# Optimization experiments

Hardware: AMD Instinct MI355X
Metric: run time of the kernel (lower is better)

Reference implementation:

```python
import jax, jax.numpy as jnp
import numpy as np
import math

B, SES, SEQ, H, K = 16, 16, 64, 512, 32
L = SES * SEQ


def setup_inputs() -> dict:
    key = jax.random.key(0)
    ks = jax.random.split(key, 16)
    s = 1.0 / math.sqrt(H)
    return {
        "user_emb": jax.random.normal(ks[0], (B, H), jnp.float32),
        "item_emb": jax.random.normal(ks[1], (B, SES, SEQ, H), jnp.float32),
        "mask": jnp.zeros((B, L, K), jnp.float32),
        "index": jax.random.randint(ks[2], (L, K), 0, L, jnp.int64),
        "Wq": jax.random.normal(ks[3], (H, H), jnp.float32) * s,
        "bq": jnp.zeros((H,), jnp.float32),
        "Wk": jax.random.normal(ks[4], (H, H), jnp.float32) * s,
        "bk": jnp.zeros((H,), jnp.float32),
        "Wv": jax.random.normal(ks[5], (H, H), jnp.float32) * s,
        "bv": jnp.zeros((H,), jnp.float32),
        "Wd": jax.random.normal(ks[6], (H, H), jnp.float32) * s,
        "bd": jnp.zeros((H,), jnp.float32),
        "ln_g": jnp.ones((H,), jnp.float32),
        "ln_b": jnp.zeros((H,), jnp.float32),
    }


def reference(user_emb, item_emb, mask, index, Wq, bq, Wk, bk, Wv, bv, Wd, bd, ln_g, ln_b):
    b, ses, seq, h = item_emb.shape
    l = ses * seq
    item_flat = item_emb.reshape(b, l, h)
    q = user_emb @ Wq.T + bq                       # [B, H]
    k = item_flat @ Wk.T + bk                      # [B, L, H]
    v = item_flat @ Wv.T + bv                      # [B, L, H]
    # scalar query against all L keys, scaled by sqrt(hidden_size)
    scores = jnp.einsum("bh,blh->bl", q, k) / math.sqrt(h)
    scores = scores[:, index] + mask               # gather -> [B, L, K]
    w = jax.nn.softmax(scores, axis=-1)            # [B, L, K]
    vg = v[:, index, :]                            # gather -> [B, L, K, H]
    attn_out = jnp.einsum("blk,blkh->blh", w, vg)  # [B, L, H]
    dense = attn_out @ Wd.T + bd
    x = dense + item_flat                          # residual (dropout = identity, eval)
    mu = jnp.mean(x, axis=-1, keepdims=True)
    var = jnp.var(x, axis=-1, keepdims=True)
    y = (x - mu) / jnp.sqrt(var + 1e-12) * ln_g + ln_b
    return y.reshape(b, ses, seq, h)
```

## Files before the change

kernel.cpp:

```cpp
#include <hip/hip_runtime.h>
#include <math.h>

constexpr int HD   = 512;
constexpr int LL   = 1024;
constexpr int MT   = 16384;
constexpr int KNBR = 32;
constexpr float SCL = 0.04419417382415922f;

typedef __attribute__((ext_vector_type(8))) short  bf16x8;
typedef __attribute__((ext_vector_type(4))) float  f32x4;

__device__ inline float b2f(unsigned short u) {
    union { unsigned int i; float f; } v; v.i = (unsigned int)u << 16; return v.f;
}
__device__ inline float b2f_lo(unsigned int u) {
    union { unsigned int i; float f; } v; v.i = u << 16; return v.f;
}
__device__ inline float b2f_hi(unsigned int u) {
    union { unsigned int i; float f; } v; v.i = u & 0xffff0000u; return v.f;
}
__device__ inline unsigned short f2b(float x) {
    union { float f; unsigned int u; } v; v.f = x;
    unsigned int r = v.u + 0x7fff + ((v.u >> 16) & 1);
    return (unsigned short)(r >> 16);
}

constexpr int PB_CONV_I = 8192;
constexpr int PB_CONV_W = 512;
constexpr int PB_Q      = 2048;

__global__ __launch_bounds__(256) void prep(
    const float* __restrict__ item, const float* __restrict__ Wv,
    const float* __restrict__ Wd, const float* __restrict__ u,
    const float* __restrict__ Wq, const float* __restrict__ bq,
    unsigned short* __restrict__ item_bf, unsigned short* __restrict__ Wv_bf,
    unsigned short* __restrict__ Wd_bf, float* __restrict__ q)
{
    const int blk = blockIdx.x, tid = threadIdx.x;

    if (blk < PB_CONV_I) {
        const int i = blk * 1024 + tid * 4;
        float4 v = *(const float4*)&item[i];
        ushort4 o;
        o.x = f2b(v.x); o.y = f2b(v.y); o.z = f2b(v.z); o.w = f2b(v.w);
        *(ushort4*)&item_bf[i] = o;
        return;
    }
    if (blk < PB_CONV_I + PB_CONV_W) {
        const int n = HD*HD;
        const int i = (blk - PB_CONV_I) * 1024 + tid * 4;
        const float* s; unsigned short* d; int off;
        if (i < n) { s = Wv; d = Wv_bf; off = i; }
        else       { s = Wd; d = Wd_bf; off = i - n; }
        float4 v = *(const float4*)&s[off];
        ushort4 o;
        o.x = f2b(v.x); o.y = f2b(v.y); o.z = f2b(v.z); o.w = f2b(v.w);
        *(ushort4*)&d[off] = o;
        return;
    }
    {
        const int wid  = (blk - PB_CONV_I - PB_CONV_W) * 4 + (tid >> 6);
        const int lane = tid & 63;
        const int b = wid >> 9, h = wid & 511;
        const float* ur = &u[b*HD + lane*8];
        const float* wr = &Wq[(size_t)h*HD + lane*8];
        const float4 u0 = *(const float4*)ur, u1 = *(const float4*)(ur+4);
        const float4 w0 = *(const float4*)wr, w1 = *(const float4*)(wr+4);
        float acc = u0.x*w0.x + u0.y*w0.y + u0.z*w0.z + u0.w*w0.w
                  + u1.x*w1.x + u1.y*w1.y + u1.z*w1.z + u1.w*w1.w;
        #pragma unroll
        for (int off = 32; off; off >>= 1) acc += __shfl_down(acc, off);
        if (lane == 0) q[b*HD + h] = acc + bq[h];
    }
}

__global__ __launch_bounds__(256) void gemm_v_r(
    const unsigned short* __restrict__ A, const unsigned short* __restrict__ W,
    const float* __restrict__ bv, const float* __restrict__ Wk,
    const float* __restrict__ bk, const float* __restrict__ q,
    unsigned short* __restrict__ v_bf, float* __restrict__ rbuf,
    float* __restrict__ s0buf)
{
    __shared__ unsigned short As[128 * 32];
    __shared__ unsigned short Bs[128 * 32];

    const int blk = blockIdx.x;
    const int tid = threadIdx.x;

    if (blk >= 512) {
        if (blk < 640) {
            __shared__ float red[4][64];
            const int rblk = blk - 512;
            const int b = rblk >> 3, c0 = (rblk & 7) * 64;
            const int cl = tid & 63, hg = tid >> 6;
            const float* qb = &q[b*HD];
            const float* wb = &Wk[(size_t)hg*128*HD + c0 + cl];
            float acc = 0.f;
            #pragma unroll 8
            for (int h = 0; h < 128; h++)
                acc += qb[hg*128 + h] * wb[(size_t)h*HD];
            red[hg][cl] = acc;
            __syncthreads();
            if (tid < 64)
                rbuf[b*HD + c0 + tid] = SCL *
                    (red[0][tid] + red[1][tid] + red[2][tid] + red[3][tid]);
        } else {
            __shared__ float sp[4];
            const int b = blk - 640;
            float p = q[b*HD + tid]*bk[tid] + q[b*HD + tid + 256]*bk[tid + 256];
            #pragma unroll
            for (int off = 32; off; off >>= 1) p += __shfl_down(p, off);
            if ((tid & 63) == 0) sp[tid >> 6] = p;
            __syncthreads();
            if (tid == 0) s0buf[b] = (sp[0] + sp[1] + sp[2] + sp[3]) * SCL;
        }
        return;
    }

    const int wave = tid >> 6, lane = tid & 63;
    const int wm = (wave >> 1) * 64;
    const int wn = (wave & 1)  * 64;
    const int row0 = (blk >> 2) * 128;
    const int col0 = (blk & 3)  * 128;

    const int lrr = lane >> 2;
    const int cc  = lane & 3;
    int st_row[2], st_gchunk[2];
    #pragma unroll
    for (int t = 0; t < 2; t++) {
        const int m = wave*32 + t*16 + lrr;
        st_row[t]    = m;
        st_gchunk[t] = cc ^ ((m >> 1) & 3);
    }

    const int fr   = lane & 15;
    const int quad = lane >> 4;

    f32x4 acc[4][4];
    #pragma unroll
    for (int i = 0; i < 4; i++)
        #pragma unroll
        for (int j = 0; j < 4; j++)
            acc[i][j] = (f32x4){0.f, 0.f, 0.f, 0.f};

    int a_off[4], b_off[4];
    #pragma unroll
    for (int i = 0; i < 4; i++) {
        const int m = wm + i*16 + fr;
        a_off[i] = m*32 + ((quad ^ ((m >> 1) & 3)) << 3);
        const int n = wn + i*16 + fr;
        b_off[i] = n*32 + ((quad ^ ((n >> 1) & 3)) << 3);
    }

    for (int k0 = 0; k0 < HD; k0 += 32) {
        #pragma unroll
        for (int t = 0; t < 2; t++) {
            const int m = st_row[t];
            const unsigned short* ga = &A[(size_t)(row0 + m)*HD + k0 + st_gchunk[t]*8];
            __builtin_amdgcn_global_load_lds(
                (const __attribute__((address_space(1))) void*)ga,
                (__attribute__((address_space(3))) void*)&As[(wave*32 + t*16)*32],
                16, 0, 0);
            const unsigned short* gw = &W[(size_t)(col0 + m)*HD + k0 + st_gchunk[t]*8];
            __builtin_amdgcn_global_load_lds(
                (const __attribute__((address_space(1))) void*)gw,
                (__attribute__((address_space(3))) void*)&Bs[(wave*32 + t*16)*32],
                16, 0, 0);
        }
        __syncthreads();

        bf16x8 af[4], bfr[4];
        #pragma unroll
        for (int i = 0; i < 4; i++) {
            af[i]  = *(const bf16x8*)&As[a_off[i]];
            bfr[i] = *(const bf16x8*)&Bs[b_off[i]];
        }
        #pragma unroll
        for (int i = 0; i < 4; i++)
            #pragma unroll
            for (int j = 0; j < 4; j++)
                acc[i][j] = __builtin_amdgcn_mfma_f32_16x16x32_bf16(
                    af[i], bfr[j], acc[i][j], 0, 0, 0);
        __syncthreads();
    }

    #pragma unroll
    for (int j = 0; j < 4; j++) {
        const int col = col0 + wn + j*16 + fr;
        const float bb = bv[col];
        #pragma unroll
        for (int i = 0; i < 4; i++) {
            #pragma unroll
            for (int r = 0; r < 4; r++) {
                const int row = row0 + wm + i*16 + quad*4 + r;
                v_bf[(size_t)row*HD + col] = f2b(acc[i][j][r] + bb);
            }
        }
    }
}

__global__ __launch_bounds__(256) void gp_scores(
    const float* __restrict__ rbuf, const float* __restrict__ s0buf,
    const unsigned short* __restrict__ item_bf, float* __restrict__ scores)
{
    const int m = blockIdx.x * 4 + (threadIdx.x >> 6);
    const int lane = threadIdx.x & 63;
    const int b = m >> 10;
    const unsigned short* ir = &item_bf[(size_t)m*HD + lane*8];
    const uint4 iv = *(const uint4*)ir;
    const float* rr = &rbuf[b*HD + lane*8];
    const float4 r0 = *(const float4*)rr;
    const float4 r1 = *(const float4*)(rr + 4);
    float acc = r0.x*b2f_lo(iv.x) + r0.y*b2f_hi(iv.x)
              + r0.z*b2f_lo(iv.y) + r0.w*b2f_hi(iv.y)
              + r1.x*b2f_lo(iv.z) + r1.y*b2f_hi(iv.z)
              + r1.z*b2f_lo(iv.w) + r1.w*b2f_hi(iv.w);
    #pragma unroll
    for (int off = 32; off; off >>= 1) acc += __shfl_down(acc, off);
    if (lane == 0) scores[m] = acc + s0buf[b];
}

__global__ __launch_bounds__(256) void gp_attn(
    const float* __restrict__ scores, const int* __restrict__ index,
    const float* __restrict__ mask, const unsigned short* __restrict__ v,
    unsigned short* __restrict__ attn)
{
    const int m = blockIdx.x * 4 + (threadIdx.x >> 6);
    const int lane = threadIdx.x & 63;
    const int b = m >> 10, l = m & 1023;

    const int t = lane & 31;
    const int idx = index[l*KNBR + t];
    const float s = scores[b*LL + idx] + mask[(size_t)m*KNBR + t];

    float mx = s;
    #pragma unroll
    for (int off = 16; off; off >>= 1) mx = fmaxf(mx, __shfl_xor(mx, off));
    const float e = __expf(s - mx);
    float sum = e;
    #pragma unroll
    for (int off = 16; off; off >>= 1) sum += __shfl_xor(sum, off);
    const float w = e / sum;

    const unsigned short* vbase = v + (size_t)(b << 10) * HD + lane*8;
    float a[8] = {};
    #pragma unroll 8
    for (int t2 = 0; t2 < KNBR; t2++) {
        const int   it = __shfl(idx, t2);
        const float wt = __shfl(w,   t2);
        const uint4 pv = *(const uint4*)(vbase + (size_t)it*HD);
        a[0] += wt * b2f_lo(pv.x); a[1] += wt * b2f_hi(pv.x);
        a[2] += wt * b2f_lo(pv.y); a[3] += wt * b2f_hi(pv.y);
        a[4] += wt * b2f_lo(pv.z); a[5] += wt * b2f_hi(pv.z);
        a[6] += wt * b2f_lo(pv.w); a[7] += wt * b2f_hi(pv.w);
    }
    uint4 o;
    o.x = (unsigned int)f2b(a[0]) | ((unsigned int)f2b(a[1]) << 16);
    o.y = (unsigned int)f2b(a[2]) | ((unsigned int)f2b(a[3]) << 16);
    o.z = (unsigned int)f2b(a[4]) | ((unsigned int)f2b(a[5]) << 16);
    o.w = (unsigned int)f2b(a[6]) | ((unsigned int)f2b(a[7]) << 16);
    *(uint4*)&attn[(size_t)m*HD + lane*8] = o;
}

__global__ __launch_bounds__(256) void dense_ln(
    const unsigned short* __restrict__ A,
    const unsigned short* __restrict__ W,
    const float* __restrict__ bd, const unsigned short* __restrict__ res,
    const float* __restrict__ ln_g, const float* __restrict__ ln_b,
    float* __restrict__ out)
{
    __shared__ unsigned short As[32 * 32];
    __shared__ unsigned short Bs[512 * 32];
    __shared__ float g_s[HD], lb_s[HD];
    __shared__ float rsum[4][32], rsq[4][32];

    const int tid  = threadIdx.x;
    const int wave = tid >> 6, lane = tid & 63;
    const int row0 = blockIdx.x * 32;

    {
        const int i = tid * 2;
        *(float2*)&g_s[i]  = *(const float2*)&ln_g[i];
        *(float2*)&lb_s[i] = *(const float2*)&ln_b[i];
    }

    const int lrr = lane >> 2;
    const int cc  = lane & 3;
    const int fr   = lane & 15;
    const int quad = lane >> 4;

    f32x4 acc[2][8];
    #pragma unroll
    for (int i = 0; i < 2; i++)
        #pragma unroll
        for (int j = 0; j < 8; j++)
            acc[i][j] = (f32x4){0.f, 0.f, 0.f, 0.f};

    int a_off[2], b_off[8];
    #pragma unroll
    for (int i = 0; i < 2; i++) {
        const int m = i*16 + fr;
        a_off[i] = m*32 + ((quad ^ ((m >> 1) & 3)) << 3);
    }
    #pragma unroll
    for (int j = 0; j < 8; j++) {
        const int n = wave*128 + j*16 + fr;
        b_off[j] = n*32 + ((quad ^ ((n >> 1) & 3)) << 3);
    }

    for (int k0 = 0; k0 < HD; k0 += 32) {
        #pragma unroll
        for (int t = 0; t < 8; t++) {
            const int n = wave*128 + t*16 + lrr;
            const int gch = cc ^ ((n >> 1) & 3);
            const unsigned short* gw = &W[(size_t)n*HD + k0 + gch*8];
            __builtin_amdgcn_global_load_lds(
                (const __attribute__((address_space(1))) void*)gw,
                (__attribute__((address_space(3))) void*)&Bs[(wave*128 + t*16)*32],
                16, 0, 0);
        }
        if (wave < 2) {
            const int m = wave*16 + lrr;
            const int gch = cc ^ ((m >> 1) & 3);
            const unsigned short* ga = &A[(size_t)(row0 + m)*HD + k0 + gch*8];
            __builtin_amdgcn_global_load_lds(
                (const __attribute__((address_space(1))) void*)ga,
                (__attribute__((address_space(3))) void*)&As[(wave*16)*32],
                16, 0, 0);
        }
        __syncthreads();

        bf16x8 af[2], bfr[8];
        #pragma unroll
        for (int i = 0; i < 2; i++) af[i] = *(const bf16x8*)&As[a_off[i]];
        #pragma unroll
        for (int j = 0; j < 8; j++) bfr[j] = *(const bf16x8*)&Bs[b_off[j]];
        #pragma unroll
        for (int i = 0; i < 2; i++)
            #pragma unroll
            for (int j = 0; j < 8; j++)
                acc[i][j] = __builtin_amdgcn_mfma_f32_16x16x32_bf16(
                    af[i], bfr[j], acc[i][j], 0, 0, 0);
        __syncthreads();
    }

    float bdv[8];
    #pragma unroll
    for (int j = 0; j < 8; j++) bdv[j] = bd[wave*128 + j*16 + fr];

    #pragma unroll
    for (int i = 0; i < 2; i++) {
        #pragma unroll
        for (int r = 0; r < 4; r++) {
            const int lrow = i*16 + quad*4 + r;
            const size_t gr = (size_t)(row0 + lrow) * HD;
            float a1 = 0.f, a2 = 0.f;
            #pragma unroll
            for (int j = 0; j < 8; j++) {
                const int col = wave*128 + j*16 + fr;
                float val = acc[i][j][r] + bdv[j] + b2f(res[gr + col]);
                acc[i][j][r] = val;
                a1 += val; a2 += val*val;
            }
            #pragma unroll
            for (int off = 1; off < 16; off <<= 1) {
                a1 += __shfl_xor(a1, off);
                a2 += __shfl_xor(a2, off);
            }
            if (fr == 0) { rsum[wave][lrow] = a1; rsq[wave][lrow] = a2; }
        }
    }
    __syncthreads();

    #pragma unroll
    for (int i = 0; i < 2; i++) {
        #pragma unroll
        for (int r = 0; r < 4; r++) {
            const int lrow = i*16 + quad*4 + r;
            const float tot  = rsum[0][lrow] + rsum[1][lrow] + rsum[2][lrow] + rsum[3][lrow];
            const float tot2 = rsq[0][lrow]  + rsq[1][lrow]  + rsq[2][lrow]  + rsq[3][lrow];
            const float mu  = tot * (1.f/HD);
            const float var = tot2 * (1.f/HD) - mu*mu;
            const float inv = rsqrtf(var + 1e-12f);
            const size_t gr = (size_t)(row0 + lrow) * HD;
            #pragma unroll
            for (int j = 0; j < 8; j++) {
                const int col = wave*128 + j*16 + fr;
                out[gr + col] = (acc[i][j][r] - mu)*inv*g_s[col] + lb_s[col];
            }
        }
    }
}

extern "C" void kernel_launch(void* const* d_in, const int* in_sizes, int n_in,
                              void* d_out, int out_size, void* d_ws, size_t ws_size,
                              hipStream_t stream) {
    const float* user_emb = (const float*)d_in[0];
    const float* item_emb = (const float*)d_in[1];
    const float* mask     = (const float*)d_in[2];
    const int*   index    = (const int*)  d_in[3];
    const float* Wq = (const float*)d_in[4];  const float* bq = (const float*)d_in[5];
    const float* Wk = (const float*)d_in[6];  const float* bk = (const float*)d_in[7];
    const float* Wv = (const float*)d_in[8];  const float* bv = (const float*)d_in[9];
    const float* Wd = (const float*)d_in[10]; const float* bd = (const float*)d_in[11];
    const float* ln_g = (const float*)d_in[12];
    const float* ln_b = (const float*)d_in[13];

    float* out = (float*)d_out;

    char* p = (char*)d_ws;
    unsigned short* item_bf = (unsigned short*)p; p += (size_t)MT*HD*2;
    unsigned short* v_bf    = (unsigned short*)p; p += (size_t)MT*HD*2;
    unsigned short* attn_bf = (unsigned short*)p; p += (size_t)MT*HD*2;
    unsigned short* Wv_bf   = (unsigned short*)p; p += (size_t)HD*HD*2;
    unsigned short* Wd_bf   = (unsigned short*)p; p += (size_t)HD*HD*2;
    float* q      = (float*)p; p += 16*HD*4;
    float* rbuf   = (float*)p; p += 16*HD*4;
    float* s0buf  = (float*)p; p += 16*4;
    float* scores = (float*)p; p += MT*4;

    prep<<<PB_CONV_I + PB_CONV_W + PB_Q, 256, 0, stream>>>(
        item_emb, Wv, Wd, user_emb, Wq, bq,
        item_bf, Wv_bf, Wd_bf, q);

    gemm_v_r<<<656, 256, 0, stream>>>(item_bf, Wv_bf, bv, Wk, bk, q,
                                      v_bf, rbuf, s0buf);

    gp_scores<<<MT/4, 256, 0, stream>>>(rbuf, s0buf, item_bf, scores);

    gp_attn<<<MT/4, 256, 0, stream>>>(scores, index, mask, v_bf, attn_bf);

    dense_ln<<<MT/32, 256, 0, stream>>>(attn_bf, Wd_bf, bd, item_bf,
                                        ln_g, ln_b, out);
}
```

Baseline: 192.4 us.

## Double-buffer GEMM LDS tiles, remap block order, widen dense_ln tile

Both bf16 GEMMs (V projection and dense+LayerNorm) now double-buffer their LDS tiles, so the next k-slice is loaded while MFMAs run on the current one, with one barrier per iteration. Block indices in gemm_v_r and gp_attn are permuted so that concurrently scheduled blocks spread across batches and row groups, which changes cache and channel locality. dense_ln now uses 512 threads on 64-row tiles, halving how often the full Wd panel is restaged per output row, and reads LN gamma/beta straight into registers. The cost is more LDS per block (about 72KB in dense_ln), which can limit occupancy.

```diff
diff --git a/kernel.cpp b/kernel.cpp
--- a/kernel.cpp
+++ b/kernel.cpp
@@ -81,8 +81,8 @@
     unsigned short* __restrict__ v_bf, float* __restrict__ rbuf,
     float* __restrict__ s0buf)
 {
-    __shared__ unsigned short As[128 * 32];
-    __shared__ unsigned short Bs[128 * 32];
+    __shared__ unsigned short As[2][128 * 32];
+    __shared__ unsigned short Bs[2][128 * 32];
 
     const int blk = blockIdx.x;
     const int tid = threadIdx.x;
@@ -117,11 +117,14 @@
         return;
     }
 
+    const int rowb = (blk & 7) | ((blk >> 5) << 3);
+    const int colb = (blk >> 3) & 3;
+    const int row0 = rowb * 128;
+    const int col0 = colb * 128;
+
     const int wave = tid >> 6, lane = tid & 63;
     const int wm = (wave >> 1) * 64;
     const int wn = (wave & 1)  * 64;
-    const int row0 = (blk >> 2) * 128;
-    const int col0 = (blk & 3)  * 128;
 
     const int lrr = lane >> 2;
     const int cc  = lane & 3;
@@ -152,28 +155,34 @@
         b_off[i] = n*32 + ((quad ^ ((n >> 1) & 3)) << 3);
     }
 
-    for (int k0 = 0; k0 < HD; k0 += 32) {
+    auto stage = [&](int bf, int k0) {
         #pragma unroll
         for (int t = 0; t < 2; t++) {
             const int m = st_row[t];
             const unsigned short* ga = &A[(size_t)(row0 + m)*HD + k0 + st_gchunk[t]*8];
             __builtin_amdgcn_global_load_lds(
                 (const __attribute__((address_space(1))) void*)ga,
-                (__attribute__((address_space(3))) void*)&As[(wave*32 + t*16)*32],
+                (__attribute__((address_space(3))) void*)&As[bf][(wave*32 + t*16)*32],
                 16, 0, 0);
             const unsigned short* gw = &W[(size_t)(col0 + m)*HD + k0 + st_gchunk[t]*8];
             __builtin_amdgcn_global_load_lds(
                 (const __attribute__((address_space(1))) void*)gw,
-                (__attribute__((address_space(3))) void*)&Bs[(wave*32 + t*16)*32],
+                (__attribute__((address_space(3))) void*)&Bs[bf][(wave*32 + t*16)*32],
                 16, 0, 0);
         }
-        __syncthreads();
+    };
+
+    stage(0, 0);
+    __syncthreads();
+    int cur = 0;
+    for (int k0 = 0; k0 < HD; k0 += 32) {
+        if (k0 + 32 < HD) stage(cur ^ 1, k0 + 32);
 
         bf16x8 af[4], bfr[4];
         #pragma unroll
         for (int i = 0; i < 4; i++) {
-            af[i]  = *(const bf16x8*)&As[a_off[i]];
-            bfr[i] = *(const bf16x8*)&Bs[b_off[i]];
+            af[i]  = *(const bf16x8*)&As[cur][a_off[i]];
+            bfr[i] = *(const bf16x8*)&Bs[cur][b_off[i]];
         }
         #pragma unroll
         for (int i = 0; i < 4; i++)
@@ -182,6 +191,7 @@
                 acc[i][j] = __builtin_amdgcn_mfma_f32_16x16x32_bf16(
                     af[i], bfr[j], acc[i][j], 0, 0, 0);
         __syncthreads();
+        cur ^= 1;
     }
 
     #pragma unroll
@@ -225,7 +235,8 @@
     const float* __restrict__ mask, const unsigned short* __restrict__ v,
     unsigned short* __restrict__ attn)
 {
-    const int m = blockIdx.x * 4 + (threadIdx.x >> 6);
+    const int bid = blockIdx.x;
+    const int m = ((bid & 7) << 11) | ((bid >> 3) << 2) | (int)(threadIdx.x >> 6);
     const int lane = threadIdx.x & 63;
     const int b = m >> 10, l = m & 1023;
 
@@ -262,102 +273,103 @@
     *(uint4*)&attn[(size_t)m*HD + lane*8] = o;
 }
 
-__global__ __launch_bounds__(256) void dense_ln(
+__global__ __launch_bounds__(512) void dense_ln(
     const unsigned short* __restrict__ A,
     const unsigned short* __restrict__ W,
     const float* __restrict__ bd, const unsigned short* __restrict__ res,
     const float* __restrict__ ln_g, const float* __restrict__ ln_b,
     float* __restrict__ out)
 {
-    __shared__ unsigned short As[32 * 32];
-    __shared__ unsigned short Bs[512 * 32];
-    __shared__ float g_s[HD], lb_s[HD];
-    __shared__ float rsum[4][32], rsq[4][32];
+    __shared__ unsigned short As[2][64 * 32];
+    __shared__ unsigned short Bs[2][512 * 32];
+    __shared__ float rsum[8][64], rsq[8][64];
 
     const int tid  = threadIdx.x;
     const int wave = tid >> 6, lane = tid & 63;
-    const int row0 = blockIdx.x * 32;
-
-    {
-        const int i = tid * 2;
-        *(float2*)&g_s[i]  = *(const float2*)&ln_g[i];
-        *(float2*)&lb_s[i] = *(const float2*)&ln_b[i];
-    }
+    const int row0 = blockIdx.x * 64;
 
     const int lrr = lane >> 2;
     const int cc  = lane & 3;
     const int fr   = lane & 15;
     const int quad = lane >> 4;
 
-    f32x4 acc[2][8];
-    #pragma unroll
-    for (int i = 0; i < 2; i++)
-        #pragma unroll
-        for (int j = 0; j < 8; j++)
+    f32x4 acc[4][4];
+    #pragma unroll
+    for (int i = 0; i < 4; i++)
+        #pragma unroll
+        for (int j = 0; j < 4; j++)
             acc[i][j] = (f32x4){0.f, 0.f, 0.f, 0.f};
 
-    int a_off[2], b_off[8];
-    #pragma unroll
-    for (int i = 0; i < 2; i++) {
+    int a_off[4], b_off[4];
+    #pragma unroll
+    for (int i = 0; i < 4; i++) {
         const int m = i*16 + fr;
         a_off[i] = m*32 + ((quad ^ ((m >> 1) & 3)) << 3);
-    }
-    #pragma unroll
-    for (int j = 0; j < 8; j++) {
-        const int n = wave*128 + j*16 + fr;
-        b_off[j] = n*32 + ((quad ^ ((n >> 1) & 3)) << 3);
-    }
-
-    for (int k0 = 0; k0 < HD; k0 += 32) {
-        #pragma unroll
-        for (int t = 0; t < 8; t++) {
-            const int n = wave*128 + t*16 + lrr;
+        const int n = wave*64 + i*16 + fr;
+        b_off[i] = n*32 + ((quad ^ ((n >> 1) & 3)) << 3);
+    }
+
+    auto stage = [&](int bf, int k0) {
+        #pragma unroll
+        for (int t = 0; t < 4; t++) {
+            const int n   = t*128 + wave*16 + lrr;
             const int gch = cc ^ ((n >> 1) & 3);
             const unsigned short* gw = &W[(size_t)n*HD + k0 + gch*8];
             __builtin_amdgcn_global_load_lds(
                 (const __attribute__((address_space(1))) void*)gw,
-                (__attribute__((address_space(3))) void*)&Bs[(wave*128 + t*16)*32],
+                (__attribute__((address_space(3))) void*)&Bs[bf][(t*128 + wave*16)*32],
                 16, 0, 0);
         }
-        if (wave < 2) {
-            const int m = wave*16 + lrr;
-            const int gch = cc ^ ((m >> 1) & 3);
-            const unsigned short* ga = &A[(size_t)(row0 + m)*HD + k0 + gch*8];
+        if (wave < 4) {
+            const int mm  = wave*16 + lrr;
+            const int gch = cc ^ ((mm >> 1) & 3);
+            const unsigned short* ga = &A[(size_t)(row0 + mm)*HD + k0 + gch*8];
             __builtin_amdgcn_global_load_lds(
                 (const __attribute__((address_space(1))) void*)ga,
-                (__attribute__((address_space(3))) void*)&As[(wave*16)*32],
+                (__attribute__((address_space(3))) void*)&As[bf][(wave*16)*32],
                 16, 0, 0);
         }
-        __syncthreads();
-
-        bf16x8 af[2], bfr[8];
-        #pragma unroll
-        for (int i = 0; i < 2; i++) af[i] = *(const bf16x8*)&As[a_off[i]];
-        #pragma unroll
-        for (int j = 0; j < 8; j++) bfr[j] = *(const bf16x8*)&Bs[b_off[j]];
-        #pragma unroll
-        for (int i = 0; i < 2; i++)
-            #pragma unroll
-            for (int j = 0; j < 8; j++)
+    };
+
+    stage(0, 0);
+    __syncthreads();
+    int cur = 0;
+    for (int k0 = 0; k0 < HD; k0 += 32) {
+        if (k0 + 32 < HD) stage(cur ^ 1, k0 + 32);
+
+        bf16x8 af[4], bfr[4];
+        #pragma unroll
+        for (int i = 0; i < 4; i++) {
+            af[i]  = *(const bf16x8*)&As[cur][a_off[i]];
+            bfr[i] = *(const bf16x8*)&Bs[cur][b_off[i]];
+        }
+        #pragma unroll
+        for (int i = 0; i < 4; i++)
+            #pragma unroll
+            for (int j = 0; j < 4; j++)
                 acc[i][j] = __builtin_amdgcn_mfma_f32_16x16x32_bf16(
                     af[i], bfr[j], acc[i][j], 0, 0, 0);
         __syncthreads();
-    }
-
-    float bdv[8];
-    #pragma unroll
-    for (int j = 0; j < 8; j++) bdv[j] = bd[wave*128 + j*16 + fr];
-
-    #pragma unroll
-    for (int i = 0; i < 2; i++) {
+        cur ^= 1;
+    }
+
+    float bdv[4], gv[4], lbv[4];
+    #pragma unroll
+    for (int j = 0; j < 4; j++) {
+        const int col = wave*64 + j*16 + fr;
+        bdv[j] = bd[col]; gv[j] = ln_g[col]; lbv[j] = ln_b[col];
+    }
+
+    #pragma unroll
+    for (int i = 0; i < 4; i++) {
         #pragma unroll
         for (int r = 0; r < 4; r++) {
             const int lrow = i*16 + quad*4 + r;
             const size_t gr = (size_t)(row0 + lrow) * HD;
             float a1 = 0.f, a2 = 0.f;
             #pragma unroll
-            for (int j = 0; j < 8; j++) {
-                const int col = wave*128 + j*16 + fr;
+            for (int j = 0; j < 4; j++) {
+                const int col = wave*64 + j*16 + fr;
                 float val = acc[i][j][r] + bdv[j] + b2f(res[gr + col]);
                 acc[i][j][r] = val;
                 a1 += val; a2 += val*val;
@@ -373,20 +385,24 @@
     __syncthreads();
 
     #pragma unroll
-    for (int i = 0; i < 2; i++) {
+    for (int i = 0; i < 4; i++) {
         #pragma unroll
         for (int r = 0; r < 4; r++) {
             const int lrow = i*16 + quad*4 + r;
-            const float tot  = rsum[0][lrow] + rsum[1][lrow] + rsum[2][lrow] + rsum[3][lrow];
-            const float tot2 = rsq[0][lrow]  + rsq[1][lrow]  + rsq[2][lrow]  + rsq[3][lrow];
+            float tot = 0.f, tot2 = 0.f;
+            #pragma unroll
+            for (int w2 = 0; w2 < 8; w2++) {
+                tot  += rsum[w2][lrow];
+                tot2 += rsq[w2][lrow];
+            }
             const float mu  = tot * (1.f/HD);
             const float var = tot2 * (1.f/HD) - mu*mu;
             const float inv = rsqrtf(var + 1e-12f);
             const size_t gr = (size_t)(row0 + lrow) * HD;
             #pragma unroll
-            for (int j = 0; j < 8; j++) {
-                const int col = wave*128 + j*16 + fr;
-                out[gr + col] = (acc[i][j][r] - mu)*inv*g_s[col] + lb_s[col];
+            for (int j = 0; j < 4; j++) {
+                const int col = wave*64 + j*16 + fr;
+                out[gr + col] = (acc[i][j][r] - mu)*inv*gv[j] + lbv[j];
             }
         }
     }
@@ -430,6 +446,6 @@
 
     gp_attn<<<MT/4, 256, 0, stream>>>(scores, index, mask, v_bf, attn_bf);
 
-    dense_ln<<<MT/32, 256, 0, stream>>>(attn_bf, Wd_bf, bd, item_bf,
+    dense_ln<<<MT/64, 512, 0, stream>>>(attn_bf, Wd_bf, bd, item_bf,
                                         ln_g, ln_b, out);
 }
```

After: 184.0 us. 4.4% less time.

## Double-buffer LDS in GEMM kernels and remap block order for locality

Applied to the files above, without the earlier changes.

Both the V-projection GEMM and the dense+LayerNorm GEMM now use two LDS buffers, so global-to-LDS loads for the next K slice are issued while MFMAs run on the current one. The dense kernel uses explicit vmcnt waits, raw barriers and setprio to control the overlap. Block index remapping in gemm_v_r and gp_attn groups blocks that share data, aiming for better L2 reuse. LN gamma/beta now go into registers instead of shared memory. The cost is doubled LDS footprint, which may lower occupancy, and hand-counted waitcnt values that depend on the exact number of outstanding loads.

```diff
diff --git a/kernel.cpp b/kernel.cpp
--- a/kernel.cpp
+++ b/kernel.cpp
@@ -81,8 +81,8 @@
     unsigned short* __restrict__ v_bf, float* __restrict__ rbuf,
     float* __restrict__ s0buf)
 {
-    __shared__ unsigned short As[128 * 32];
-    __shared__ unsigned short Bs[128 * 32];
+    __shared__ unsigned short As[2][128 * 32];
+    __shared__ unsigned short Bs[2][128 * 32];
 
     const int blk = blockIdx.x;
     const int tid = threadIdx.x;
@@ -117,11 +117,14 @@
         return;
     }
 
+    const int rowb = (blk & 7) | ((blk >> 5) << 3);
+    const int colb = (blk >> 3) & 3;
+    const int row0 = rowb * 128;
+    const int col0 = colb * 128;
+
     const int wave = tid >> 6, lane = tid & 63;
     const int wm = (wave >> 1) * 64;
     const int wn = (wave & 1)  * 64;
-    const int row0 = (blk >> 2) * 128;
-    const int col0 = (blk & 3)  * 128;
 
     const int lrr = lane >> 2;
     const int cc  = lane & 3;
@@ -152,28 +155,34 @@
         b_off[i] = n*32 + ((quad ^ ((n >> 1) & 3)) << 3);
     }
 
-    for (int k0 = 0; k0 < HD; k0 += 32) {
+    auto stage = [&](int bf, int k0) {
         #pragma unroll
         for (int t = 0; t < 2; t++) {
             const int m = st_row[t];
             const unsigned short* ga = &A[(size_t)(row0 + m)*HD + k0 + st_gchunk[t]*8];
             __builtin_amdgcn_global_load_lds(
                 (const __attribute__((address_space(1))) void*)ga,
-                (__attribute__((address_space(3))) void*)&As[(wave*32 + t*16)*32],
+                (__attribute__((address_space(3))) void*)&As[bf][(wave*32 + t*16)*32],
                 16, 0, 0);
             const unsigned short* gw = &W[(size_t)(col0 + m)*HD + k0 + st_gchunk[t]*8];
             __builtin_amdgcn_global_load_lds(
                 (const __attribute__((address_space(1))) void*)gw,
-                (__attribute__((address_space(3))) void*)&Bs[(wave*32 + t*16)*32],
+                (__attribute__((address_space(3))) void*)&Bs[bf][(wave*32 + t*16)*32],
                 16, 0, 0);
         }
-        __syncthreads();
+    };
+
+    stage(0, 0);
+    __syncthreads();
+    int cur = 0;
+    for (int k0 = 0; k0 < HD; k0 += 32) {
+        if (k0 + 32 < HD) stage(cur ^ 1, k0 + 32);
 
         bf16x8 af[4], bfr[4];
         #pragma unroll
         for (int i = 0; i < 4; i++) {
-            af[i]  = *(const bf16x8*)&As[a_off[i]];
-            bfr[i] = *(const bf16x8*)&Bs[b_off[i]];
+            af[i]  = *(const bf16x8*)&As[cur][a_off[i]];
+            bfr[i] = *(const bf16x8*)&Bs[cur][b_off[i]];
         }
         #pragma unroll
         for (int i = 0; i < 4; i++)
@@ -182,6 +191,7 @@
                 acc[i][j] = __builtin_amdgcn_mfma_f32_16x16x32_bf16(
                     af[i], bfr[j], acc[i][j], 0, 0, 0);
         __syncthreads();
+        cur ^= 1;
     }
 
     #pragma unroll
@@ -225,7 +235,8 @@
     const float* __restrict__ mask, const unsigned short* __restrict__ v,
     unsigned short* __restrict__ attn)
 {
-    const int m = blockIdx.x * 4 + (threadIdx.x >> 6);
+    const int bid = blockIdx.x;
+    const int m = ((bid & 7) << 11) | ((bid >> 3) << 2) | (int)(threadIdx.x >> 6);
     const int lane = threadIdx.x & 63;
     const int b = m >> 10, l = m & 1023;
 
@@ -269,20 +280,13 @@
     const float* __restrict__ ln_g, const float* __restrict__ ln_b,
     float* __restrict__ out)
 {
-    __shared__ unsigned short As[32 * 32];
-    __shared__ unsigned short Bs[512 * 32];
-    __shared__ float g_s[HD], lb_s[HD];
+    __shared__ unsigned short As[2][32 * 32];
+    __shared__ unsigned short Bs[2][512 * 32];
     __shared__ float rsum[4][32], rsq[4][32];
 
     const int tid  = threadIdx.x;
     const int wave = tid >> 6, lane = tid & 63;
     const int row0 = blockIdx.x * 32;
-
-    {
-        const int i = tid * 2;
-        *(float2*)&g_s[i]  = *(const float2*)&ln_g[i];
-        *(float2*)&lb_s[i] = *(const float2*)&ln_b[i];
-    }
 
     const int lrr = lane >> 2;
     const int cc  = lane & 3;
@@ -308,45 +312,66 @@
         b_off[j] = n*32 + ((quad ^ ((n >> 1) & 3)) << 3);
     }
 
-    for (int k0 = 0; k0 < HD; k0 += 32) {
+    auto stage = [&](int bf, int k0) {
         #pragma unroll
         for (int t = 0; t < 8; t++) {
-            const int n = wave*128 + t*16 + lrr;
+            const int n   = wave*128 + t*16 + lrr;
             const int gch = cc ^ ((n >> 1) & 3);
             const unsigned short* gw = &W[(size_t)n*HD + k0 + gch*8];
             __builtin_amdgcn_global_load_lds(
                 (const __attribute__((address_space(1))) void*)gw,
-                (__attribute__((address_space(3))) void*)&Bs[(wave*128 + t*16)*32],
+                (__attribute__((address_space(3))) void*)&Bs[bf][(wave*128 + t*16)*32],
                 16, 0, 0);
         }
         if (wave < 2) {
-            const int m = wave*16 + lrr;
-            const int gch = cc ^ ((m >> 1) & 3);
-            const unsigned short* ga = &A[(size_t)(row0 + m)*HD + k0 + gch*8];
+            const int mm  = wave*16 + lrr;
+            const int gch = cc ^ ((mm >> 1) & 3);
+            const unsigned short* ga = &A[(size_t)(row0 + mm)*HD + k0 + gch*8];
             __builtin_amdgcn_global_load_lds(
                 (const __attribute__((address_space(1))) void*)ga,
-                (__attribute__((address_space(3))) void*)&As[(wave*16)*32],
+                (__attribute__((address_space(3))) void*)&As[bf][(wave*16)*32],
                 16, 0, 0);
         }
-        __syncthreads();
-
+    };
+
+    stage(0, 0);
+    stage(1, 32);
+
+    for (int s = 0; s < 16; ++s) {
+        if (wave < 2) asm volatile("s_waitcnt vmcnt(9)" ::: "memory");
+        else          asm volatile("s_waitcnt vmcnt(8)" ::: "memory");
+        __builtin_amdgcn_s_barrier();
+        asm volatile("" ::: "memory");
+
+        const int cur = s & 1;
         bf16x8 af[2], bfr[8];
         #pragma unroll
-        for (int i = 0; i < 2; i++) af[i] = *(const bf16x8*)&As[a_off[i]];
-        #pragma unroll
-        for (int j = 0; j < 8; j++) bfr[j] = *(const bf16x8*)&Bs[b_off[j]];
+        for (int i = 0; i < 2; i++) af[i] = *(const bf16x8*)&As[cur][a_off[i]];
+        #pragma unroll
+        for (int j = 0; j < 8; j++) bfr[j] = *(const bf16x8*)&Bs[cur][b_off[j]];
+        asm volatile("s_waitcnt lgkmcnt(0)" ::: "memory");
+        __builtin_amdgcn_sched_barrier(0);
+        __builtin_amdgcn_s_barrier();
+
+        if (s + 2 < 16) stage(cur, (s + 2) * 32);
+
+        __builtin_amdgcn_s_setprio(1);
         #pragma unroll
         for (int i = 0; i < 2; i++)
             #pragma unroll
             for (int j = 0; j < 8; j++)
                 acc[i][j] = __builtin_amdgcn_mfma_f32_16x16x32_bf16(
                     af[i], bfr[j], acc[i][j], 0, 0, 0);
-        __syncthreads();
-    }
-
-    float bdv[8];
-    #pragma unroll
-    for (int j = 0; j < 8; j++) bdv[j] = bd[wave*128 + j*16 + fr];
+        __builtin_amdgcn_s_setprio(0);
+    }
+    __syncthreads();
+
+    float bdv[8], gv[8], lbv[8];
+    #pragma unroll
+    for (int j = 0; j < 8; j++) {
+        const int col = wave*128 + j*16 + fr;
+        bdv[j] = bd[col]; gv[j] = ln_g[col]; lbv[j] = ln_b[col];
+    }
 
     #pragma unroll
     for (int i = 0; i < 2; i++) {
@@ -386,7 +411,7 @@
             #pragma unroll
             for (int j = 0; j < 8; j++) {
                 const int col = wave*128 + j*16 + fr;
-                out[gr + col] = (acc[i][j][r] - mu)*inv*g_s[col] + lb_s[col];
+                out[gr + col] = (acc[i][j][r] - mu)*inv*gv[j] + lbv[j];
             }
         }
     }
```

Result: faster. 184.5 us (-4.1%).
